# Performance work log

Hardware: AMD Instinct MI355X
Metric: run time of the kernel (lower is better)

The kernel has to match this reference:

```python
import jax, jax.numpy as jnp
import numpy as np

B, T, D, H = 4, 2048, 1024, 16
HD = D // H  # head_dim = 64

def setup_inputs() -> dict:
    key = jax.random.key(0)
    k1, k2, k3 = jax.random.split(key, 3)
    s = 1.0 / np.sqrt(D)
    return {
        "x": jax.random.normal(k1, (B, T, D), dtype=jnp.float32),
        "w_qkv": jax.random.normal(k2, (D, 3 * D), dtype=jnp.float32) * s,
        "b_qkv": jnp.zeros((3 * D,), dtype=jnp.float32),
        "w_proj": jax.random.normal(k3, (D, D), dtype=jnp.float32) * s,
        "b_proj": jnp.zeros((D,), dtype=jnp.float32),
    }

def reference(x, w_qkv, b_qkv, w_proj, b_proj):
    b, t, c = x.shape
    qkv = x @ w_qkv + b_qkv                       # [B,T,3D]
    qkv = qkv.reshape(b, t, 3, H, HD)
    q, k, v = (jnp.transpose(qkv[:, :, i], (0, 2, 1, 3)) for i in range(3))  # [B,H,T,HD]
    scale = 1.0 / np.sqrt(HD)
    attn = jnp.einsum('bhqd,bhkd->bhqk', q, k) * scale  # [B,H,T,T]
    attn = jax.nn.softmax(attn, axis=-1)
    out = jnp.einsum('bhqk,bhkd->bhqd', attn, v)        # [B,H,T,HD]
    out = jnp.transpose(out, (0, 2, 1, 3)).reshape(b, t, c)
    return out @ w_proj + b_proj
```

## Files before the change

### kernel.cpp

```cpp
#include <hip/hip_runtime.h>
#include <hip/hip_bf16.h>

#define T_SEQ   2048
#define D_MODEL 1024
#define N_HEADS 16
#define HEAD_DIM 64
#define BT      8192
#define N3D     3072

using short8  = __attribute__((ext_vector_type(8))) short;
using short4v = __attribute__((ext_vector_type(4))) short;
using floatx4 = __attribute__((ext_vector_type(4))) float;

#define QSCALE 0.18033688f

__device__ __forceinline__ unsigned short rne_bf16(float f) {
  unsigned int u = __float_as_uint(f);
  u = (u + 0x7fffu + ((u >> 16) & 1u)) >> 16;
  return (unsigned short)u;
}

__device__ __forceinline__ void gload_lds16(const unsigned short* g,
                                            unsigned short* l) {
  __builtin_amdgcn_global_load_lds(
      (const __attribute__((address_space(1))) void*)g,
      (__attribute__((address_space(3))) void*)l, 16, 0, 0);
}

__global__ __launch_bounds__(256) void k_convert(const float* __restrict__ in,
                                                 unsigned short* __restrict__ out) {
  size_t i = ((size_t)blockIdx.x * 256 + threadIdx.x) * 8;
  float4 a = *(const float4*)(in + i);
  float4 b = *(const float4*)(in + i + 4);
  short8 v;
  v[0] = (short)rne_bf16(a.x); v[1] = (short)rne_bf16(a.y);
  v[2] = (short)rne_bf16(a.z); v[3] = (short)rne_bf16(a.w);
  v[4] = (short)rne_bf16(b.x); v[5] = (short)rne_bf16(b.y);
  v[6] = (short)rne_bf16(b.z); v[7] = (short)rne_bf16(b.w);
  *(short8*)(((short*)out) + i) = v;
}

__global__ __launch_bounds__(256) void k_transpose_convert(
    const float* __restrict__ in, unsigned short* __restrict__ out_hi,
    int R, int C) {
  __shared__ float tile[64][65];
  int tiles_c = C >> 6;
  int r0 = (blockIdx.x / tiles_c) << 6;
  int c0 = (blockIdx.x % tiles_c) << 6;
  int tid = threadIdx.x;
#pragma unroll
  for (int i = 0; i < 16; ++i) {
    int idx = tid + i * 256;
    int r = idx >> 6, c = idx & 63;
    tile[r][c] = in[(size_t)(r0 + r) * C + c0 + c];
  }
  __syncthreads();
#pragma unroll
  for (int i = 0; i < 16; ++i) {
    int idx = tid + i * 256;
    int orow = idx >> 6, oc = idx & 63;
    out_hi[(size_t)(c0 + orow) * R + r0 + oc] = rne_bf16(tile[oc][orow]);
  }
}

__global__ __launch_bounds__(256) void k_qkv_gemm(
    const unsigned short* __restrict__ A, const unsigned short* __restrict__ Bt,
    const float* __restrict__ bias,
    unsigned short* __restrict__ Qo, unsigned short* __restrict__ Ko,
    unsigned short* __restrict__ Vt) {
  __shared__ __align__(16) unsigned short As[128 * 32];
  __shared__ __align__(16) unsigned short Bs[128 * 32];
  int tid = threadIdx.x;
  int m0 = (blockIdx.x / 24) * 128;
  int n0 = (blockIdx.x % 24) * 128;
  int w = tid >> 6, lane = tid & 63, quad = lane >> 4, l16 = lane & 15;
  int wm = (w >> 1) * 64, wn = (w & 1) * 64;
  floatx4 acc[4][4] = {};

  int s_row[2], s_sp[2];
#pragma unroll
  for (int i = 0; i < 2; ++i) {
    int u = tid + i * 256;
    s_row[i] = u >> 2;
    s_sp[i] = (u & 3) ^ ((s_row[i] >> 1) & 3);
  }
  int a_off[4], b_off[4];
#pragma unroll
  for (int t = 0; t < 4; ++t) {
    int ra = wm + t * 16 + l16, rb = wn + t * 16 + l16;
    a_off[t] = ra * 32 + (quad ^ ((ra >> 1) & 3)) * 8;
    b_off[t] = rb * 32 + (quad ^ ((rb >> 1) & 3)) * 8;
  }

  for (int k0 = 0; k0 < 1024; k0 += 32) {
#pragma unroll
    for (int i = 0; i < 2; ++i) {
      int ub = (tid & ~63) + i * 256;
      gload_lds16(A + (size_t)(m0 + s_row[i]) * 1024 + k0 + s_sp[i] * 8,
                  &As[ub * 8]);
      gload_lds16(Bt + (size_t)(n0 + s_row[i]) * 1024 + k0 + s_sp[i] * 8,
                  &Bs[ub * 8]);
    }
    __syncthreads();
    short8 af[4], bf[4];
#pragma unroll
    for (int mt = 0; mt < 4; ++mt) af[mt] = *(const short8*)(&As[a_off[mt]]);
#pragma unroll
    for (int nt = 0; nt < 4; ++nt) bf[nt] = *(const short8*)(&Bs[b_off[nt]]);
#pragma unroll
    for (int mt = 0; mt < 4; ++mt)
#pragma unroll
      for (int nt = 0; nt < 4; ++nt)
        acc[mt][nt] = __builtin_amdgcn_mfma_f32_16x16x32_bf16(af[mt], bf[nt],
                                                              acc[mt][nt], 0, 0, 0);
    __syncthreads();
  }

#pragma unroll
  for (int nt = 0; nt < 4; ++nt) {
    int n = n0 + wn + nt * 16 + l16;
    float bv = bias[n];
    int which = n >> 10;
    int nn = n & 1023;
    int h = nn >> 6, hd = nn & 63;
#pragma unroll
    for (int mt = 0; mt < 4; ++mt) {
      int mbase = m0 + wm + mt * 16 + quad * 4;
      int b = mbase >> 11;
      int t0 = mbase & 2047;
      int head = b * N_HEADS + h;
      if (which == 2) {
        short4v vv;
#pragma unroll
        for (int r = 0; r < 4; ++r) vv[r] = (short)rne_bf16(acc[mt][nt][r] + bv);
        *(short4v*)(&Vt[((size_t)head * HEAD_DIM + hd) * T_SEQ + t0]) = vv;
      } else {
        unsigned short* dst = (which == 0) ? Qo : Ko;
        float scl = (which == 0) ? QSCALE : 1.0f;
#pragma unroll
        for (int r = 0; r < 4; ++r)
          dst[((size_t)head * T_SEQ + t0 + r) * HEAD_DIM + hd] =
              rne_bf16((acc[mt][nt][r] + bv) * scl);
      }
    }
  }
}

__global__ __launch_bounds__(256) void k_attn(
    const unsigned short* __restrict__ Q, const unsigned short* __restrict__ K,
    const unsigned short* __restrict__ Vt, unsigned short* __restrict__ Oo) {
  __shared__ __align__(16) unsigned short Klds[64 * 64];
  __shared__ __align__(16) unsigned short Vlds[64 * 64];
  int tid = threadIdx.x;
  int head = blockIdx.x >> 4;
  int qb = (blockIdx.x & 15) << 7;
  int b = head >> 4, h = head & 15;
  int w = tid >> 6, lane = tid & 63, quad = lane >> 4, l16 = lane & 15;
  const unsigned short* Qh = Q + (size_t)head * T_SEQ * HEAD_DIM;
  const unsigned short* Kh = K + (size_t)head * T_SEQ * HEAD_DIM;
  const unsigned short* Vh = Vt + (size_t)head * HEAD_DIM * T_SEQ;

  short8 qf[2][2];
#pragma unroll
  for (int qi = 0; qi < 2; ++qi) {
    int qrow = qb + w * 32 + qi * 16 + l16;
#pragma unroll
    for (int ks = 0; ks < 2; ++ks)
      qf[qi][ks] = *(const short8*)(Qh + (size_t)qrow * 64 + ks * 32 + quad * 8);
  }

  short8 ones;
#pragma unroll
  for (int j = 0; j < 8; ++j) ones[j] = (short)0x3F80;

  floatx4 O[2][4] = {};
  floatx4 Osum[2] = {};
  const floatx4 zf = {};

  int sg[2], sub[2], ksrc[2], vsrc[2];
#pragma unroll
  for (int i = 0; i < 2; ++i) {
    sg[i] = (tid + i * 256) >> 6;
    sub[i] = (tid & ~63) + i * 256;
    int xs = lane ^ sg[i];
    int ntp = xs >> 4, mp = xs & 15;
    ksrc[i] = ((ntp >> 1) << 5) + ((mp >> 2) << 3) + ((ntp & 1) << 2) + (mp & 3);
    vsrc[i] = xs;
  }

  for (int kb = 0; kb < 32; ++kb) {
#pragma unroll
    for (int i = 0; i < 2; ++i) {
      gload_lds16(Kh + ((size_t)(kb * 64 + ksrc[i])) * 64 + sg[i] * 8,
                  &Klds[sub[i] * 8]);
      gload_lds16(Vh + (size_t)vsrc[i] * T_SEQ + kb * 64 + sg[i] * 8,
                  &Vlds[sub[i] * 8]);
    }
    __syncthreads();

    floatx4 s[2][4];
#pragma unroll
    for (int ks = 0; ks < 2; ++ks) {
      int gk = ks * 4 + quad;
#pragma unroll
      for (int nt = 0; nt < 4; ++nt) {
        int PU = ((gk << 6) + nt * 16 + l16) ^ gk;
        short8 kf = *(const short8*)(&Klds[PU * 8]);
        if (ks == 0) {
          s[0][nt] = __builtin_amdgcn_mfma_f32_16x16x32_bf16(kf, qf[0][0], zf, 0, 0, 0);
          s[1][nt] = __builtin_amdgcn_mfma_f32_16x16x32_bf16(kf, qf[1][0], zf, 0, 0, 0);
        } else {
          s[0][nt] = __builtin_amdgcn_mfma_f32_16x16x32_bf16(kf, qf[0][1], s[0][nt], 0, 0, 0);
          s[1][nt] = __builtin_amdgcn_mfma_f32_16x16x32_bf16(kf, qf[1][1], s[1][nt], 0, 0, 0);
        }
      }
    }

    short8 pB[2][2];
#pragma unroll
    for (int qi = 0; qi < 2; ++qi) {
      unsigned int dw[4][2];
#pragma unroll
      for (int nt = 0; nt < 4; ++nt) {
        float p0 = __builtin_amdgcn_exp2f(s[qi][nt][0]);
        float p1 = __builtin_amdgcn_exp2f(s[qi][nt][1]);
        float p2 = __builtin_amdgcn_exp2f(s[qi][nt][2]);
        float p3 = __builtin_amdgcn_exp2f(s[qi][nt][3]);
        __hip_bfloat162 lo2 = __float22bfloat162_rn(make_float2(p0, p1));
        __hip_bfloat162 hi2 = __float22bfloat162_rn(make_float2(p2, p3));
        dw[nt][0] = *(unsigned int*)&lo2;
        dw[nt][1] = *(unsigned int*)&hi2;
      }
#pragma unroll
      for (int ks = 0; ks < 2; ++ks) {
        union { unsigned int u[4]; short8 s8; } cv;
        cv.u[0] = dw[2 * ks][0];
        cv.u[1] = dw[2 * ks][1];
        cv.u[2] = dw[2 * ks + 1][0];
        cv.u[3] = dw[2 * ks + 1][1];
        pB[qi][ks] = cv.s8;
      }
    }

#pragma unroll
    for (int ks = 0; ks < 2; ++ks) {
      int gk = ks * 4 + quad;
      Osum[0] = __builtin_amdgcn_mfma_f32_16x16x32_bf16(ones, pB[0][ks], Osum[0], 0, 0, 0);
      Osum[1] = __builtin_amdgcn_mfma_f32_16x16x32_bf16(ones, pB[1][ks], Osum[1], 0, 0, 0);
#pragma unroll
      for (int dt = 0; dt < 4; ++dt) {
        int PUv = ((gk << 6) + dt * 16 + l16) ^ gk;
        short8 vf = *(const short8*)(&Vlds[PUv * 8]);
        O[0][dt] = __builtin_amdgcn_mfma_f32_16x16x32_bf16(vf, pB[0][ks], O[0][dt], 0, 0, 0);
        O[1][dt] = __builtin_amdgcn_mfma_f32_16x16x32_bf16(vf, pB[1][ks], O[1][dt], 0, 0, 0);
      }
    }
    __syncthreads();
  }

#pragma unroll
  for (int qi = 0; qi < 2; ++qi) {
    float inv = 1.0f / Osum[qi][0];
    int t = qb + w * 32 + qi * 16 + l16;
    size_t rowo = ((size_t)(b * T_SEQ + t)) * D_MODEL + h * HEAD_DIM;
#pragma unroll
    for (int dt = 0; dt < 4; ++dt) {
      short4v ov;
#pragma unroll
      for (int r = 0; r < 4; ++r) ov[r] = (short)rne_bf16(O[qi][dt][r] * inv);
      *(short4v*)(&Oo[rowo + dt * 16 + quad * 4]) = ov;
    }
  }
}

__global__ __launch_bounds__(256) void k_proj_gemm(
    const unsigned short* __restrict__ A, const unsigned short* __restrict__ Bt,
    const float* __restrict__ bias, float* __restrict__ out) {
  __shared__ __align__(16) unsigned short As[128 * 32];
  __shared__ __align__(16) unsigned short Bs[128 * 32];
  int tid = threadIdx.x;
  int m0 = (blockIdx.x >> 3) * 128;
  int n0 = (blockIdx.x & 7) * 128;
  int w = tid >> 6, lane = tid & 63, quad = lane >> 4, l16 = lane & 15;
  int wm = (w >> 1) * 64, wn = (w & 1) * 64;
  floatx4 acc[4][4] = {};

  int s_row[2], s_sp[2];
#pragma unroll
  for (int i = 0; i < 2; ++i) {
    int u = tid + i * 256;
    s_row[i] = u >> 2;
    s_sp[i] = (u & 3) ^ ((s_row[i] >> 1) & 3);
  }
  int a_off[4], b_off[4];
#pragma unroll
  for (int t = 0; t < 4; ++t) {
    int ra = wm + t * 16 + l16, rb = wn + t * 16 + l16;
    a_off[t] = ra * 32 + (quad ^ ((ra >> 1) & 3)) * 8;
    b_off[t] = rb * 32 + (quad ^ ((rb >> 1) & 3)) * 8;
  }

  for (int k0 = 0; k0 < 1024; k0 += 32) {
#pragma unroll
    for (int i = 0; i < 2; ++i) {
      int ub = (tid & ~63) + i * 256;
      gload_lds16(A + (size_t)(m0 + s_row[i]) * 1024 + k0 + s_sp[i] * 8,
                  &As[ub * 8]);
      gload_lds16(Bt + (size_t)(n0 + s_row[i]) * 1024 + k0 + s_sp[i] * 8,
                  &Bs[ub * 8]);
    }
    __syncthreads();
    short8 af[4], bf[4];
#pragma unroll
    for (int mt = 0; mt < 4; ++mt) af[mt] = *(const short8*)(&As[a_off[mt]]);
#pragma unroll
    for (int nt = 0; nt < 4; ++nt) bf[nt] = *(const short8*)(&Bs[b_off[nt]]);
#pragma unroll
    for (int mt = 0; mt < 4; ++mt)
#pragma unroll
      for (int nt = 0; nt < 4; ++nt)
        acc[mt][nt] = __builtin_amdgcn_mfma_f32_16x16x32_bf16(af[mt], bf[nt],
                                                              acc[mt][nt], 0, 0, 0);
    __syncthreads();
  }

#pragma unroll
  for (int nt = 0; nt < 4; ++nt) {
    int n = n0 + wn + nt * 16 + l16;
    float bv = bias[n];
#pragma unroll
    for (int mt = 0; mt < 4; ++mt)
#pragma unroll
      for (int r = 0; r < 4; ++r) {
        int m = m0 + wm + mt * 16 + quad * 4 + r;
        out[(size_t)m * 1024 + n] = acc[mt][nt][r] + bv;
      }
  }
}

extern "C" void kernel_launch(void* const* d_in, const int* in_sizes, int n_in,
                              void* d_out, int out_size, void* d_ws, size_t ws_size,
                              hipStream_t stream) {
  const float* x     = (const float*)d_in[0];
  const float* wqkv  = (const float*)d_in[1];
  const float* bqkv  = (const float*)d_in[2];
  const float* wproj = (const float*)d_in[3];
  const float* bproj = (const float*)d_in[4];

  char* ws = (char*)d_ws;
  size_t off = 0;
  unsigned short* x_bf  = (unsigned short*)(ws + off); off += (size_t)BT * D_MODEL * 2;
  unsigned short* wq_T  = (unsigned short*)(ws + off); off += (size_t)N3D * D_MODEL * 2;
  unsigned short* wp_T  = (unsigned short*)(ws + off); off += (size_t)D_MODEL * D_MODEL * 2;
  unsigned short* Qb    = (unsigned short*)(ws + off); off += (size_t)BT * D_MODEL * 2;
  unsigned short* Kb    = (unsigned short*)(ws + off); off += (size_t)BT * D_MODEL * 2;
  unsigned short* Vt    = (unsigned short*)(ws + off); off += (size_t)BT * D_MODEL * 2;
  unsigned short* a_bf  = (unsigned short*)(ws + off); off += (size_t)BT * D_MODEL * 2;

  k_convert<<<(BT * D_MODEL) / (256 * 8), 256, 0, stream>>>(x, x_bf);
  k_transpose_convert<<<(1024 / 64) * (3072 / 64), 256, 0, stream>>>(wqkv, wq_T, 1024, 3072);
  k_transpose_convert<<<(1024 / 64) * (1024 / 64), 256, 0, stream>>>(wproj, wp_T, 1024, 1024);
  k_qkv_gemm<<<(BT / 128) * (N3D / 128), 256, 0, stream>>>(x_bf, wq_T, bqkv, Qb, Kb, Vt);
  k_attn<<<(T_SEQ / 128) * 4 * N_HEADS, 256, 0, stream>>>(Qb, Kb, Vt, a_bf);
  k_proj_gemm<<<(BT / 128) * (D_MODEL / 128), 256, 0, stream>>>(a_bf, wp_T, bproj, (float*)d_out);
}
```

Before: 325.4 us.

## Load K and V fragments directly from global memory in attention, dropping LDS staging

The attention kernel no longer stages K and V tiles through shared memory with swizzled async loads and barriers. Each wave now reads its MFMA operand fragments straight from global memory, relying on the cache, and the two workgroup barriers per key block are removed. The cost is that all four waves redundantly fetch the same K/V data from L2/L1 and the loads are less coalesced. The fragment loads are also interleaved with the MFMA chains, trying to hide their latency without any explicit prefetch.

```diff
diff --git a/kernel.cpp b/kernel.cpp
--- a/kernel.cpp
+++ b/kernel.cpp
@@ -149,8 +149,6 @@
 __global__ __launch_bounds__(256) void k_attn(
     const unsigned short* __restrict__ Q, const unsigned short* __restrict__ K,
     const unsigned short* __restrict__ Vt, unsigned short* __restrict__ Oo) {
-  __shared__ __align__(16) unsigned short Klds[64 * 64];
-  __shared__ __align__(16) unsigned short Vlds[64 * 64];
   int tid = threadIdx.x;
   int head = blockIdx.x >> 4;
   int qb = (blockIdx.x & 15) << 7;
@@ -177,44 +175,36 @@
   floatx4 Osum[2] = {};
   const floatx4 zf = {};
 
-  int sg[2], sub[2], ksrc[2], vsrc[2];
-#pragma unroll
-  for (int i = 0; i < 2; ++i) {
-    sg[i] = (tid + i * 256) >> 6;
-    sub[i] = (tid & ~63) + i * 256;
-    int xs = lane ^ sg[i];
-    int ntp = xs >> 4, mp = xs & 15;
-    ksrc[i] = ((ntp >> 1) << 5) + ((mp >> 2) << 3) + ((ntp & 1) << 2) + (mp & 3);
-    vsrc[i] = xs;
-  }
-
-  for (int kb = 0; kb < 32; ++kb) {
-#pragma unroll
-    for (int i = 0; i < 2; ++i) {
-      gload_lds16(Kh + ((size_t)(kb * 64 + ksrc[i])) * 64 + sg[i] * 8,
-                  &Klds[sub[i] * 8]);
-      gload_lds16(Vh + (size_t)vsrc[i] * T_SEQ + kb * 64 + sg[i] * 8,
-                  &Vlds[sub[i] * 8]);
-    }
-    __syncthreads();
+  int kperm = ((l16 >> 2) << 3) + (l16 & 3);
+  int kcol = quad * 8;
+  const unsigned short* Kp = Kh + (size_t)kperm * 64 + kcol;
+  const unsigned short* Vp = Vh + (size_t)l16 * T_SEQ + quad * 8;
+
+  for (int kb = 0; kb < 32; ++kb, Kp += 64 * 64, Vp += 64) {
+    short8 kf0[4], kf1[4];
+#pragma unroll
+    for (int nt = 0; nt < 4; ++nt) {
+      int knt = ((nt >> 1) << 5) + ((nt & 1) << 2);
+      kf0[nt] = *(const short8*)(Kp + (size_t)knt * 64);
+      kf1[nt] = *(const short8*)(Kp + (size_t)knt * 64 + 32);
+    }
 
     floatx4 s[2][4];
 #pragma unroll
-    for (int ks = 0; ks < 2; ++ks) {
-      int gk = ks * 4 + quad;
-#pragma unroll
-      for (int nt = 0; nt < 4; ++nt) {
-        int PU = ((gk << 6) + nt * 16 + l16) ^ gk;
-        short8 kf = *(const short8*)(&Klds[PU * 8]);
-        if (ks == 0) {
-          s[0][nt] = __builtin_amdgcn_mfma_f32_16x16x32_bf16(kf, qf[0][0], zf, 0, 0, 0);
-          s[1][nt] = __builtin_amdgcn_mfma_f32_16x16x32_bf16(kf, qf[1][0], zf, 0, 0, 0);
-        } else {
-          s[0][nt] = __builtin_amdgcn_mfma_f32_16x16x32_bf16(kf, qf[0][1], s[0][nt], 0, 0, 0);
-          s[1][nt] = __builtin_amdgcn_mfma_f32_16x16x32_bf16(kf, qf[1][1], s[1][nt], 0, 0, 0);
-        }
-      }
-    }
+    for (int nt = 0; nt < 4; ++nt) {
+      s[0][nt] = __builtin_amdgcn_mfma_f32_16x16x32_bf16(kf0[nt], qf[0][0], zf, 0, 0, 0);
+      s[1][nt] = __builtin_amdgcn_mfma_f32_16x16x32_bf16(kf0[nt], qf[1][0], zf, 0, 0, 0);
+    }
+#pragma unroll
+    for (int nt = 0; nt < 4; ++nt) {
+      s[0][nt] = __builtin_amdgcn_mfma_f32_16x16x32_bf16(kf1[nt], qf[0][1], s[0][nt], 0, 0, 0);
+      s[1][nt] = __builtin_amdgcn_mfma_f32_16x16x32_bf16(kf1[nt], qf[1][1], s[1][nt], 0, 0, 0);
+    }
+
+    short8 vf0[4];
+#pragma unroll
+    for (int dt = 0; dt < 4; ++dt)
+      vf0[dt] = *(const short8*)(Vp + (size_t)(dt * 16) * T_SEQ);
 
     short8 pB[2][2];
 #pragma unroll
@@ -242,20 +232,26 @@
       }
     }
 
-#pragma unroll
-    for (int ks = 0; ks < 2; ++ks) {
-      int gk = ks * 4 + quad;
-      Osum[0] = __builtin_amdgcn_mfma_f32_16x16x32_bf16(ones, pB[0][ks], Osum[0], 0, 0, 0);
-      Osum[1] = __builtin_amdgcn_mfma_f32_16x16x32_bf16(ones, pB[1][ks], Osum[1], 0, 0, 0);
-#pragma unroll
-      for (int dt = 0; dt < 4; ++dt) {
-        int PUv = ((gk << 6) + dt * 16 + l16) ^ gk;
-        short8 vf = *(const short8*)(&Vlds[PUv * 8]);
-        O[0][dt] = __builtin_amdgcn_mfma_f32_16x16x32_bf16(vf, pB[0][ks], O[0][dt], 0, 0, 0);
-        O[1][dt] = __builtin_amdgcn_mfma_f32_16x16x32_bf16(vf, pB[1][ks], O[1][dt], 0, 0, 0);
-      }
-    }
-    __syncthreads();
+    Osum[0] = __builtin_amdgcn_mfma_f32_16x16x32_bf16(ones, pB[0][0], Osum[0], 0, 0, 0);
+    Osum[1] = __builtin_amdgcn_mfma_f32_16x16x32_bf16(ones, pB[1][0], Osum[1], 0, 0, 0);
+#pragma unroll
+    for (int dt = 0; dt < 4; ++dt) {
+      O[0][dt] = __builtin_amdgcn_mfma_f32_16x16x32_bf16(vf0[dt], pB[0][0], O[0][dt], 0, 0, 0);
+      O[1][dt] = __builtin_amdgcn_mfma_f32_16x16x32_bf16(vf0[dt], pB[1][0], O[1][dt], 0, 0, 0);
+    }
+
+    short8 vf1[4];
+#pragma unroll
+    for (int dt = 0; dt < 4; ++dt)
+      vf1[dt] = *(const short8*)(Vp + (size_t)(dt * 16) * T_SEQ + 32);
+
+    Osum[0] = __builtin_amdgcn_mfma_f32_16x16x32_bf16(ones, pB[0][1], Osum[0], 0, 0, 0);
+    Osum[1] = __builtin_amdgcn_mfma_f32_16x16x32_bf16(ones, pB[1][1], Osum[1], 0, 0, 0);
+#pragma unroll
+    for (int dt = 0; dt < 4; ++dt) {
+      O[0][dt] = __builtin_amdgcn_mfma_f32_16x16x32_bf16(vf1[dt], pB[0][1], O[0][dt], 0, 0, 0);
+      O[1][dt] = __builtin_amdgcn_mfma_f32_16x16x32_bf16(vf1[dt], pB[1][1], O[1][dt], 0, 0, 0);
+    }
   }
 
 #pragma unroll
```

New measurement: 484.7 us. 1.49x slower.
